# Performance work log

Hardware: AMD Instinct MI355X
Metric: run time of the kernel (lower is better)

The kernel has to match this reference:

```python
import jax, jax.numpy as jnp
import numpy as np

C_IN = 512      # backbone feature dim (din)
CORR = 256      # cfg.SIAMESE.NUM_CHANNELS_FOR_CORRELATION
EXPAND = 64     # expand_factor
N_ANCH = 9      # 3 scales x 3 ratios
KH = 7          # template spatial size
H = W = 32      # target feature map size
N_T = 2         # number of templates
BN_EPS = 1e-5


def _conv(x, w, b=None, pad=0, groups=1):
    out = jax.lax.conv_general_dilated(
        x, w, window_strides=(1, 1), padding=[(pad, pad), (pad, pad)],
        dimension_numbers=('NCHW', 'OIHW', 'NCHW'), feature_group_count=groups)
    if b is not None:
        out = out + b[None, :, None, None]
    return out


def setup_inputs() -> dict:
    key = jax.random.key(0)
    ks = jax.random.split(key, 10)
    return {
        'target_feat': jax.random.normal(ks[0], (1, C_IN, H, W), jnp.float32),
        'template_feat': jax.random.normal(ks[1], (N_T, C_IN, KH, KH), jnp.float32),
        'w_target': jax.random.normal(ks[2], (CORR, C_IN, 3, 3), jnp.float32) * 0.01,
        'b_target': jnp.zeros((CORR,), jnp.float32),
        'bn_gamma': jnp.ones((CORR,), jnp.float32),
        'bn_beta': jnp.zeros((CORR,), jnp.float32),
        'bn_mean': jax.random.normal(ks[3], (CORR,), jnp.float32) * 0.1,
        'bn_var': jax.random.uniform(ks[4], (CORR,), jnp.float32, 0.5, 1.5),
        'w_template': jax.random.normal(ks[5], (CORR * EXPAND, C_IN, 3, 3), jnp.float32) * 0.01,
        'b_template': jnp.zeros((CORR * EXPAND,), jnp.float32),
        'w_merge_cls': jax.random.normal(ks[6], (CORR,), jnp.float32) * 0.01,
        'corr_bias': jnp.zeros((EXPAND, 1, 1), jnp.float32),
        'w_cls': jax.random.normal(ks[7], (2 * N_ANCH, EXPAND, 1, 1), jnp.float32) * 0.01,
        'b_cls': jnp.zeros((2 * N_ANCH,), jnp.float32),
        'w_box': jax.random.normal(ks[8], (4 * N_ANCH, EXPAND, 1, 1), jnp.float32) * 0.001,
        'b_box': jnp.zeros((4 * N_ANCH,), jnp.float32),
    }


def reference(target_feat, template_feat, w_target, b_target, bn_gamma, bn_beta,
              bn_mean, bn_var, w_template, b_template, w_merge_cls, corr_bias,
              w_cls, b_cls, w_box, b_box):
    N = template_feat.shape[0]
    Hh, Ww = target_feat.shape[2], target_feat.shape[3]
    # RPN_Conv_target (3x3, pad 1) + BatchNorm (eval mode, running stats)
    t = _conv(target_feat, w_target, b_target, pad=1)               # (1, CORR, H, W)
    scale = (bn_gamma / jnp.sqrt(bn_var + BN_EPS))[None, :, None, None]
    t = (t - bn_mean[None, :, None, None]) * scale + bn_beta[None, :, None, None]
    # RPN_Conv_template (3x3, pad 1) on template features
    z = _conv(template_feat, w_template, b_template, pad=1)          # (N, CORR*EXPAND, kh, kw)
    kh, kw = z.shape[2], z.shape[3]
    # depth-wise cross correlation: kernel (N*EXPAND*CORR, 1, kh, kw), groups=CORR
    kern = z.reshape(N * EXPAND * CORR, 1, kh, kw)
    out = 0.1 * _conv(t, kern, pad=(kh - 1) // 2, groups=CORR)       # (1, N*EXPAND*CORR, H, W)
    out = out.reshape(N * EXPAND, CORR, Hh, Ww)
    # conv_merge_1x1_cls: 1x1 conv CORR -> 1, no bias
    out = jnp.einsum('nchw,c->nhw', out, w_merge_cls)                # (N*EXPAND, H, W)
    rpn_feat = out.reshape(N, EXPAND, Hh, Ww) + corr_bias[None]      # (N, 64, H, W)
    # cls / bbox heads (1x1 convs)
    cls = _conv(rpn_feat, w_cls, b_cls)                              # (N, 18, H, W)
    box = _conv(rpn_feat, w_box, b_box)                              # (N, 36, H, W)
    nc = cls.shape[1]
    # reshape to (N, 2, A*H, W), softmax over dim 1, reshape back
    prob = jax.nn.softmax(cls.reshape(N, 2, (nc // 2) * Hh, Ww), axis=1)
    prob = prob.reshape(N, nc, Hh, Ww)
    return prob, box
```

## Files before the change

### kernel.cpp

```cpp
#include <hip/hip_runtime.h>
#include <math.h>


#define WS_TFP 0
#define WS_WT  591872
#define WS_TP  1771520
#define WS_WF  2160640
#define WS_BF  2750464
#define WS_Z2P 2750592
#define WS_MRG 3152000

typedef float f4u __attribute__((ext_vector_type(4), aligned(4)));

__global__ __launch_bounds__(256) void k_fold(
    const float* __restrict__ wtpl,
    const float* __restrict__ wm,
    float* ws)
{
  const int g = blockIdx.x / 9, chunk = blockIdx.x % 9;
  const int tid = threadIdx.x;
  const int t = tid & 127, grp = tid >> 7;
  const int c0 = chunk * 512 + t * 4;
  const float* base = wtpl + (size_t)(g * 128 + grp * 64) * 4608 + c0;
  const float* wmb = wm + (g & 1) * 128 + grp * 64;
  float4 acc = make_float4(0.f, 0.f, 0.f, 0.f);
  for (int r = 0; r < 64; r += 8) {
    const float4 v0 = *(const float4*)(base + (size_t)(r + 0) * 4608);
    const float4 v1 = *(const float4*)(base + (size_t)(r + 1) * 4608);
    const float4 v2 = *(const float4*)(base + (size_t)(r + 2) * 4608);
    const float4 v3 = *(const float4*)(base + (size_t)(r + 3) * 4608);
    const float4 v4 = *(const float4*)(base + (size_t)(r + 4) * 4608);
    const float4 v5 = *(const float4*)(base + (size_t)(r + 5) * 4608);
    const float4 v6 = *(const float4*)(base + (size_t)(r + 6) * 4608);
    const float4 v7 = *(const float4*)(base + (size_t)(r + 7) * 4608);
    const float w0 = wmb[r + 0], w1 = wmb[r + 1], w2 = wmb[r + 2], w3 = wmb[r + 3];
    const float w4 = wmb[r + 4], w5 = wmb[r + 5], w6 = wmb[r + 6], w7 = wmb[r + 7];
    acc.x = fmaf(w0, v0.x, acc.x); acc.y = fmaf(w0, v0.y, acc.y);
    acc.z = fmaf(w0, v0.z, acc.z); acc.w = fmaf(w0, v0.w, acc.w);
    acc.x = fmaf(w1, v1.x, acc.x); acc.y = fmaf(w1, v1.y, acc.y);
    acc.z = fmaf(w1, v1.z, acc.z); acc.w = fmaf(w1, v1.w, acc.w);
    acc.x = fmaf(w2, v2.x, acc.x); acc.y = fmaf(w2, v2.y, acc.y);
    acc.z = fmaf(w2, v2.z, acc.z); acc.w = fmaf(w2, v2.w, acc.w);
    acc.x = fmaf(w3, v3.x, acc.x); acc.y = fmaf(w3, v3.y, acc.y);
    acc.z = fmaf(w3, v3.z, acc.z); acc.w = fmaf(w3, v3.w, acc.w);
    acc.x = fmaf(w4, v4.x, acc.x); acc.y = fmaf(w4, v4.y, acc.y);
    acc.z = fmaf(w4, v4.z, acc.z); acc.w = fmaf(w4, v4.w, acc.w);
    acc.x = fmaf(w5, v5.x, acc.x); acc.y = fmaf(w5, v5.y, acc.y);
    acc.z = fmaf(w5, v5.z, acc.z); acc.w = fmaf(w5, v5.w, acc.w);
    acc.x = fmaf(w6, v6.x, acc.x); acc.y = fmaf(w6, v6.y, acc.y);
    acc.z = fmaf(w6, v6.z, acc.z); acc.w = fmaf(w6, v6.w, acc.w);
    acc.x = fmaf(w7, v7.x, acc.x); acc.y = fmaf(w7, v7.y, acc.y);
    acc.z = fmaf(w7, v7.z, acc.z); acc.w = fmaf(w7, v7.w, acc.w);
  }
  __shared__ float4 red[128];
  if (grp) red[t] = acc;
  __syncthreads();
  if (!grp) {
    const float4 o = red[t];
    acc.x += o.x; acc.y += o.y; acc.z += o.z; acc.w += o.w;
    float* wf = ws + WS_WF;
    wf[(size_t)(c0 + 0) * 128 + g] = acc.x;
    wf[(size_t)(c0 + 1) * 128 + g] = acc.y;
    wf[(size_t)(c0 + 2) * 128 + g] = acc.z;
    wf[(size_t)(c0 + 3) * 128 + g] = acc.w;
  }
}

__global__ __launch_bounds__(256) void k0_prep(
    const float* __restrict__ tfeat,
    const float* __restrict__ wm,
    const float* __restrict__ btpl,
    float* ws)
{
  const int N0 = 591872, N2 = 389120;
  const int total = N0 + N2;
  for (int idx = blockIdx.x * 256 + threadIdx.x; idx < total + 128; idx += gridDim.x * 256) {
    if (idx < N0) {
      int ci = idx / 1156, r = idx % 1156;
      int yy = r / 34, xx = r % 34;
      float v = 0.f;
      if (yy >= 1 && yy <= 32 && xx >= 1 && xx <= 32)
        v = tfeat[ci * 1024 + (yy - 1) * 32 + (xx - 1)];
      ws[WS_TFP + idx] = v;
    } else if (idx < total) {
      ws[WS_TP + (idx - N0)] = 0.f;
    } else {
      const int eh = idx - total;
      const int e = eh >> 1, h = eh & 1;
      const float* wmp = wm + h * 128;
      const float* bp = btpl + e * 256 + h * 128;
      float s = 0.f;
      for (int cl = 0; cl < 128; cl++) s = fmaf(wmp[cl], bp[cl], s);
      ws[WS_BF + eh] = s;
    }
  }
}

__global__ __launch_bounds__(512) void k_conv(
    const float* __restrict__ wtgt,
    const float* __restrict__ btgt,
    const float* __restrict__ gamma, const float* __restrict__ beta,
    const float* __restrict__ mean, const float* __restrict__ var,
    float* ws)
{
  __shared__ float red[3][128][8];
  const int tid = threadIdx.x;
  const int ks = tid >> 7;
  const int sub = tid & 127;
  const int cog = sub >> 5;
  const int pxg = sub & 31;
  const int row = pxg >> 4;
  const int x0 = (pxg & 15) * 2;
  const int co0 = (blockIdx.x >> 4) * 16 + cog * 4;
  const int y = (blockIdx.x & 15) * 2 + row;
  const float* tfp = ws + WS_TFP;

  float acc[4][2] = {{0.f, 0.f}, {0.f, 0.f}, {0.f, 0.f}, {0.f, 0.f}};
  for (int i = 0; i < 128; i++) {
    const int ci = ks * 128 + i;
    const float* tin = tfp + (size_t)ci * 1156 + y * 34 + x0;
    const f4u p0 = *(const f4u*)(tin);
    const f4u p1 = *(const f4u*)(tin + 34);
    const f4u p2 = *(const f4u*)(tin + 68);
    #pragma unroll
    for (int c = 0; c < 4; c++) {
      const float* wr = wtgt + (size_t)(co0 + c) * 4608 + ci * 9;
      const f4u wa = *(const f4u*)(wr);
      const f4u wb = *(const f4u*)(wr + 4);
      const float w8 = wr[8];
      acc[c][0] += wa.x * p0.x + wa.y * p0.y + wa.z * p0.z
                 + wa.w * p1.x + wb.x * p1.y + wb.y * p1.z
                 + wb.z * p2.x + wb.w * p2.y + w8 * p2.z;
      acc[c][1] += wa.x * p0.y + wa.y * p0.z + wa.z * p0.w
                 + wa.w * p1.y + wb.x * p1.z + wb.y * p1.w
                 + wb.z * p2.y + wb.w * p2.z + w8 * p2.w;
    }
  }
  if (ks) {
    #pragma unroll
    for (int c = 0; c < 4; c++) {
      red[ks - 1][sub][c * 2 + 0] = acc[c][0];
      red[ks - 1][sub][c * 2 + 1] = acc[c][1];
    }
  }
  __syncthreads();
  if (ks == 0) {
    float* tP = ws + WS_TP;
    #pragma unroll
    for (int c = 0; c < 4; c++) {
      const int co = co0 + c;
      const float sc = gamma[co] * rsqrtf(var[co] + 1e-5f);
      #pragma unroll
      for (int p = 0; p < 2; p++) {
        float a = acc[c][p] + red[0][sub][c * 2 + p]
                            + red[1][sub][c * 2 + p]
                            + red[2][sub][c * 2 + p];
        float t = (a + btgt[co] - mean[co]) * sc + beta[co];
        t *= 0.1f;
        tP[co * 1520 + (y + 3) * 40 + (x0 + p + 3)] = t;
      }
    }
  }
}

__global__ __launch_bounds__(256) void k2_z2(
    const float* __restrict__ zfeat,
    float* ws)
{
  __shared__ float Tl[50][144];
  const int tid = threadIdx.x;
  const int n = blockIdx.x >> 5, kc = blockIdx.x & 31;
  const int ci0 = kc * 16;
  for (int idx = tid; idx < 7200; idx += 256) {
    const int uv = idx / 144, kk = idx % 144;
    float v = 0.f;
    if (uv < 49) {
      const int u = uv / 7, vv = uv % 7;
      const int ci = ci0 + kk / 9, pq = kk % 9;
      const int p = pq / 3, q = pq % 3;
      const int yy = u + p - 1, xx = vv + q - 1;
      if (yy >= 0 && yy < 7 && xx >= 0 && xx < 7)
        v = zfeat[n * 25088 + ci * 49 + yy * 7 + xx];
    }
    Tl[uv][kk] = v;
  }
  __syncthreads();
  const int ehq = tid & 31, uvg = tid >> 5;
  const int eh0 = ehq * 4;
  const int uv0 = (uvg == 0) ? 0 : uvg * 6 + 1;
  const float* wf = ws + WS_WF;
  float4 acc[7];
  #pragma unroll
  for (int i = 0; i < 7; i++) acc[i] = make_float4(0.f, 0.f, 0.f, 0.f);
  for (int g = 0; g < 36; g++) {
    const float* wr = wf + (size_t)(ci0 * 9 + g * 4) * 128 + eh0;
    const float4 wv0 = *(const float4*)(wr);
    const float4 wv1 = *(const float4*)(wr + 128);
    const float4 wv2 = *(const float4*)(wr + 256);
    const float4 wv3 = *(const float4*)(wr + 384);
    #pragma unroll
    for (int uu = 0; uu < 7; uu++) {
      const float4 t4 = *(const float4*)(&Tl[uv0 + uu][g * 4]);
      acc[uu].x = fmaf(t4.x, wv0.x, fmaf(t4.y, wv1.x, fmaf(t4.z, wv2.x, fmaf(t4.w, wv3.x, acc[uu].x))));
      acc[uu].y = fmaf(t4.x, wv0.y, fmaf(t4.y, wv1.y, fmaf(t4.z, wv2.y, fmaf(t4.w, wv3.y, acc[uu].y))));
      acc[uu].z = fmaf(t4.x, wv0.z, fmaf(t4.y, wv1.z, fmaf(t4.z, wv2.z, fmaf(t4.w, wv3.z, acc[uu].z))));
      acc[uu].w = fmaf(t4.x, wv0.w, fmaf(t4.y, wv1.w, fmaf(t4.z, wv2.w, fmaf(t4.w, wv3.w, acc[uu].w))));
    }
  }
  float* z2p = ws + WS_Z2P;
  #pragma unroll
  for (int uu = 0; uu < 7; uu++) {
    const int uv = uv0 + uu;
    if (uv <= 48)
      *(float4*)(z2p + ((size_t)((n * 32 + kc) * 49 + uv)) * 128 + eh0) = acc[uu];
  }
}

__global__ __launch_bounds__(128) void k3_merged(float* ws)
{
  __shared__ float Z2s[16][7][8];
  const int tid = threadIdx.x;
  const int bid = blockIdx.x;
  const int n = bid >> 7, rest = bid & 127;
  const int ec = rest >> 4, hq = rest & 15;
  const int c0 = ec * 16, h0 = hq * 2;
  const float* z2p = ws + WS_Z2P;
  const float* bf = ws + WS_BF;
  for (int idx = tid; idx < 784; idx += 128) {
    const int cl = idx & 15, uv = idx >> 4;
    float s = bf[c0 + cl];
    const float* p = z2p + (size_t)(n * 1568 + uv) * 128 + (c0 + cl);
    #pragma unroll 8
    for (int kc = 0; kc < 32; kc++) s += p[(size_t)kc * 6272];
    Z2s[cl][uv / 7][uv % 7] = s;
  }
  for (int idx = tid; idx < 112; idx += 128)
    Z2s[idx / 7][idx % 7][7] = 0.f;
  __syncthreads();

  const int e = tid >> 4, row = (tid >> 3) & 1, wq = tid & 7;
  const int w0 = wq * 4;
  const float* tP = ws + WS_TP;
  float acc[4] = {0.f, 0.f, 0.f, 0.f};
  #pragma unroll
  for (int h128 = 0; h128 < 2; h128++) {
    const int cl = 2 * e + h128;
    const float* tc = tP + (size_t)(128 * n + c0 + cl) * 1520;
    #pragma unroll
    for (int u = 0; u < 7; u++) {
      const float* trow = tc + (h0 + row + u) * 40 + w0;
      float tw[12];
      *(float4*)&tw[0] = *(const float4*)(trow);
      *(float4*)&tw[4] = *(const float4*)(trow + 4);
      *(float4*)&tw[8] = *(const float4*)(trow + 8);
      float z[8];
      *(float4*)&z[0] = *(const float4*)&Z2s[cl][u][0];
      *(float4*)&z[4] = *(const float4*)&Z2s[cl][u][4];
      #pragma unroll
      for (int px = 0; px < 4; px++)
        #pragma unroll
        for (int v = 0; v < 8; v++)
          acc[px] = fmaf(z[v], tw[px + v], acc[px]);
    }
  }
  float* mrg = ws + WS_MRG;
  *(float4*)(mrg + (size_t)(((n * 64 + ec * 8 + e) * 32) + h0 + row) * 32 + w0) =
      make_float4(acc[0], acc[1], acc[2], acc[3]);
}

__global__ __launch_bounds__(256) void k4_heads(
    const float* __restrict__ cb,
    const float* __restrict__ wcls, const float* __restrict__ bcls,
    const float* __restrict__ wbox, const float* __restrict__ bbox,
    float* ws, float* __restrict__ out)
{
  __shared__ float mrg_l[32][66];
  __shared__ float wcb_l[54][64];
  __shared__ float bias_l[54];
  __shared__ float logits[18][32];
  const int tid = threadIdx.x;
  const int n = blockIdx.x >> 5, h = blockIdx.x & 31;
  const float* mrg = ws + WS_MRG;
  for (int idx = tid; idx < 2048; idx += 256) {
    const int e = idx >> 5, w = idx & 31;
    mrg_l[w][e] = mrg[(size_t)(((n * 64 + e) * 32) + h) * 32 + w] + cb[e];
  }
  for (int idx = tid; idx < 3456; idx += 256) {
    const int ch = idx >> 6, e = idx & 63;
    wcb_l[ch][e] = (ch < 18) ? wcls[ch * 64 + e] : wbox[(ch - 18) * 64 + e];
  }
  if (tid < 54) bias_l[tid] = (tid < 18) ? bcls[tid] : bbox[tid - 18];
  __syncthreads();

  const int w = tid & 31, chg = tid >> 5;
  const int cnt = (chg < 6) ? 7 : 6;
  float acc[7] = {0.f, 0.f, 0.f, 0.f, 0.f, 0.f, 0.f};
  for (int e2 = 0; e2 < 32; e2++) {
    const float2 m2 = *(const float2*)&mrg_l[w][e2 * 2];
    #pragma unroll
    for (int i = 0; i < 7; i++) {
      if (i < cnt) {
        const int ch = chg + 8 * i;
        const float2 wv = *(const float2*)&wcb_l[ch][e2 * 2];
        acc[i] = fmaf(m2.x, wv.x, acc[i]);
        acc[i] = fmaf(m2.y, wv.y, acc[i]);
      }
    }
  }
  #pragma unroll
  for (int i = 0; i < 7; i++) {
    if (i < cnt) {
      const int ch = chg + 8 * i;
      const float v = acc[i] + bias_l[ch];
      if (ch < 18) logits[ch][w] = v;
      else out[36864 + n * 36864 + (ch - 18) * 1024 + h * 32 + w] = v;
    }
  }
  __syncthreads();
  for (int idx = tid; idx < 576; idx += 256) {
    const int ch = idx >> 5, w2 = idx & 31;
    const float a = logits[ch][w2];
    const float b = logits[(ch + 9) % 18][w2];
    const float m = fmaxf(a, b);
    const float ea = expf(a - m), eb = expf(b - m);
    out[n * 18432 + ch * 1024 + h * 32 + w2] = ea / (ea + eb);
  }
}

extern "C" void kernel_launch(void* const* d_in, const int* in_sizes, int n_in,
                              void* d_out, int out_size, void* d_ws, size_t ws_size,
                              hipStream_t stream) {
  (void)in_sizes; (void)n_in; (void)out_size; (void)ws_size;
  const float* target_feat   = (const float*)d_in[0];
  const float* template_feat = (const float*)d_in[1];
  const float* w_target      = (const float*)d_in[2];
  const float* b_target      = (const float*)d_in[3];
  const float* bn_gamma      = (const float*)d_in[4];
  const float* bn_beta       = (const float*)d_in[5];
  const float* bn_mean       = (const float*)d_in[6];
  const float* bn_var        = (const float*)d_in[7];
  const float* w_template    = (const float*)d_in[8];
  const float* b_template    = (const float*)d_in[9];
  const float* w_merge       = (const float*)d_in[10];
  const float* corr_bias     = (const float*)d_in[11];
  const float* w_cls         = (const float*)d_in[12];
  const float* b_cls         = (const float*)d_in[13];
  const float* w_box         = (const float*)d_in[14];
  const float* b_box         = (const float*)d_in[15];
  float* ws = (float*)d_ws;
  float* out = (float*)d_out;

  hipLaunchKernelGGL(k_fold, dim3(1152), dim3(256), 0, stream,
                     w_template, w_merge, ws);
  hipLaunchKernelGGL(k0_prep, dim3(2048), dim3(256), 0, stream,
                     target_feat, w_merge, b_template, ws);
  hipLaunchKernelGGL(k_conv, dim3(256), dim3(512), 0, stream,
                     w_target, b_target, bn_gamma, bn_beta, bn_mean, bn_var, ws);
  hipLaunchKernelGGL(k2_z2, dim3(64), dim3(256), 0, stream,
                     template_feat, ws);
  hipLaunchKernelGGL(k3_merged, dim3(256), dim3(128), 0, stream, ws);
  hipLaunchKernelGGL(k4_heads, dim3(64), dim3(256), 0, stream,
                     corr_bias, w_cls, b_cls, w_box, b_box, ws, out);
}
```

Before: 231.5 us.

## Split-K the target conv and template fold across more blocks with partial-sum buffers

The target 3x3 conv moves from 256 blocks, each reducing all 512 input channels, to 2048 blocks that each handle a 64-channel slice. Partials go to 16 global buffers, and a new k_cred kernel sums them and applies BatchNorm. k_fold is likewise split into two row halves written to separate buffers, which k2_z2 adds together on load. The aim is better GPU occupancy for work that was under-parallelized, at the cost of extra global partial-sum traffic and one more kernel launch.

```diff
diff --git a/kernel.cpp b/kernel.cpp
--- a/kernel.cpp
+++ b/kernel.cpp
@@ -3,66 +3,78 @@
 
 
 #define WS_TFP 0
-#define WS_WT  591872
-#define WS_TP  1771520
-#define WS_WF  2160640
-#define WS_BF  2750464
-#define WS_Z2P 2750592
-#define WS_MRG 3152000
+#define WS_TP  591872
+#define WS_BF  980992
+#define WS_WFP 981120
+#define WS_Z2P 2160768
+#define WS_MRG 2562176
+#define WS_CVP 2693248
+#define WFP_HALF 589824
 
 typedef float f4u __attribute__((ext_vector_type(4), aligned(4)));
+
+#define FMA4(ww, vv) \
+  acc.x = fmaf(ww, (vv).x, acc.x); acc.y = fmaf(ww, (vv).y, acc.y); \
+  acc.z = fmaf(ww, (vv).z, acc.z); acc.w = fmaf(ww, (vv).w, acc.w)
 
 __global__ __launch_bounds__(256) void k_fold(
     const float* __restrict__ wtpl,
     const float* __restrict__ wm,
     float* ws)
 {
-  const int g = blockIdx.x / 9, chunk = blockIdx.x % 9;
-  const int tid = threadIdx.x;
-  const int t = tid & 127, grp = tid >> 7;
-  const int c0 = chunk * 512 + t * 4;
-  const float* base = wtpl + (size_t)(g * 128 + grp * 64) * 4608 + c0;
-  const float* wmb = wm + (g & 1) * 128 + grp * 64;
+  const int bid = blockIdx.x;
+  const int g = bid / 18, rest = bid % 18;
+  const int chunk = rest >> 1, half = rest & 1;
+  const int tid = threadIdx.x;
+  const int colv = tid & 127, rowg = tid >> 7;
+  const int c0 = chunk * 512 + colv * 4;
+  const int row0 = g * 128 + half * 64 + rowg * 32;
+  const float* base = wtpl + (size_t)row0 * 4608 + c0;
+  const float* wmb = wm + (g & 1) * 128 + half * 64 + rowg * 32;
   float4 acc = make_float4(0.f, 0.f, 0.f, 0.f);
-  for (int r = 0; r < 64; r += 8) {
-    const float4 v0 = *(const float4*)(base + (size_t)(r + 0) * 4608);
-    const float4 v1 = *(const float4*)(base + (size_t)(r + 1) * 4608);
-    const float4 v2 = *(const float4*)(base + (size_t)(r + 2) * 4608);
-    const float4 v3 = *(const float4*)(base + (size_t)(r + 3) * 4608);
-    const float4 v4 = *(const float4*)(base + (size_t)(r + 4) * 4608);
-    const float4 v5 = *(const float4*)(base + (size_t)(r + 5) * 4608);
-    const float4 v6 = *(const float4*)(base + (size_t)(r + 6) * 4608);
-    const float4 v7 = *(const float4*)(base + (size_t)(r + 7) * 4608);
-    const float w0 = wmb[r + 0], w1 = wmb[r + 1], w2 = wmb[r + 2], w3 = wmb[r + 3];
-    const float w4 = wmb[r + 4], w5 = wmb[r + 5], w6 = wmb[r + 6], w7 = wmb[r + 7];
-    acc.x = fmaf(w0, v0.x, acc.x); acc.y = fmaf(w0, v0.y, acc.y);
-    acc.z = fmaf(w0, v0.z, acc.z); acc.w = fmaf(w0, v0.w, acc.w);
-    acc.x = fmaf(w1, v1.x, acc.x); acc.y = fmaf(w1, v1.y, acc.y);
-    acc.z = fmaf(w1, v1.z, acc.z); acc.w = fmaf(w1, v1.w, acc.w);
-    acc.x = fmaf(w2, v2.x, acc.x); acc.y = fmaf(w2, v2.y, acc.y);
-    acc.z = fmaf(w2, v2.z, acc.z); acc.w = fmaf(w2, v2.w, acc.w);
-    acc.x = fmaf(w3, v3.x, acc.x); acc.y = fmaf(w3, v3.y, acc.y);
-    acc.z = fmaf(w3, v3.z, acc.z); acc.w = fmaf(w3, v3.w, acc.w);
-    acc.x = fmaf(w4, v4.x, acc.x); acc.y = fmaf(w4, v4.y, acc.y);
-    acc.z = fmaf(w4, v4.z, acc.z); acc.w = fmaf(w4, v4.w, acc.w);
-    acc.x = fmaf(w5, v5.x, acc.x); acc.y = fmaf(w5, v5.y, acc.y);
-    acc.z = fmaf(w5, v5.z, acc.z); acc.w = fmaf(w5, v5.w, acc.w);
-    acc.x = fmaf(w6, v6.x, acc.x); acc.y = fmaf(w6, v6.y, acc.y);
-    acc.z = fmaf(w6, v6.z, acc.z); acc.w = fmaf(w6, v6.w, acc.w);
-    acc.x = fmaf(w7, v7.x, acc.x); acc.y = fmaf(w7, v7.y, acc.y);
-    acc.z = fmaf(w7, v7.z, acc.z); acc.w = fmaf(w7, v7.w, acc.w);
+  #pragma unroll
+  for (int rr = 0; rr < 32; rr += 16) {
+    const float* b = base + (size_t)rr * 4608;
+    const float4 v0  = *(const float4*)(b);
+    const float4 v1  = *(const float4*)(b + 1 * 4608);
+    const float4 v2  = *(const float4*)(b + 2 * 4608);
+    const float4 v3  = *(const float4*)(b + 3 * 4608);
+    const float4 v4  = *(const float4*)(b + 4 * 4608);
+    const float4 v5  = *(const float4*)(b + 5 * 4608);
+    const float4 v6  = *(const float4*)(b + 6 * 4608);
+    const float4 v7  = *(const float4*)(b + 7 * 4608);
+    const float4 v8  = *(const float4*)(b + 8 * 4608);
+    const float4 v9  = *(const float4*)(b + 9 * 4608);
+    const float4 v10 = *(const float4*)(b + 10 * 4608);
+    const float4 v11 = *(const float4*)(b + 11 * 4608);
+    const float4 v12 = *(const float4*)(b + 12 * 4608);
+    const float4 v13 = *(const float4*)(b + 13 * 4608);
+    const float4 v14 = *(const float4*)(b + 14 * 4608);
+    const float4 v15 = *(const float4*)(b + 15 * 4608);
+    const float w0 = wmb[rr + 0],  w1 = wmb[rr + 1];
+    const float w2 = wmb[rr + 2],  w3 = wmb[rr + 3];
+    const float w4 = wmb[rr + 4],  w5 = wmb[rr + 5];
+    const float w6 = wmb[rr + 6],  w7 = wmb[rr + 7];
+    const float w8 = wmb[rr + 8],  w9 = wmb[rr + 9];
+    const float w10 = wmb[rr + 10], w11 = wmb[rr + 11];
+    const float w12 = wmb[rr + 12], w13 = wmb[rr + 13];
+    const float w14 = wmb[rr + 14], w15 = wmb[rr + 15];
+    FMA4(w0, v0);   FMA4(w1, v1);   FMA4(w2, v2);   FMA4(w3, v3);
+    FMA4(w4, v4);   FMA4(w5, v5);   FMA4(w6, v6);   FMA4(w7, v7);
+    FMA4(w8, v8);   FMA4(w9, v9);   FMA4(w10, v10); FMA4(w11, v11);
+    FMA4(w12, v12); FMA4(w13, v13); FMA4(w14, v14); FMA4(w15, v15);
   }
   __shared__ float4 red[128];
-  if (grp) red[t] = acc;
-  __syncthreads();
-  if (!grp) {
-    const float4 o = red[t];
+  if (rowg) red[colv] = acc;
+  __syncthreads();
+  if (!rowg) {
+    const float4 o = red[colv];
     acc.x += o.x; acc.y += o.y; acc.z += o.z; acc.w += o.w;
-    float* wf = ws + WS_WF;
-    wf[(size_t)(c0 + 0) * 128 + g] = acc.x;
-    wf[(size_t)(c0 + 1) * 128 + g] = acc.y;
-    wf[(size_t)(c0 + 2) * 128 + g] = acc.z;
-    wf[(size_t)(c0 + 3) * 128 + g] = acc.w;
+    float* wp = ws + WS_WFP + (size_t)half * WFP_HALF;
+    wp[(size_t)(c0 + 0) * 128 + g] = acc.x;
+    wp[(size_t)(c0 + 1) * 128 + g] = acc.y;
+    wp[(size_t)(c0 + 2) * 128 + g] = acc.z;
+    wp[(size_t)(c0 + 3) * 128 + g] = acc.w;
   }
 }
 
@@ -96,28 +108,24 @@
   }
 }
 
-__global__ __launch_bounds__(512) void k_conv(
+__global__ __launch_bounds__(256) void k_conv(
     const float* __restrict__ wtgt,
-    const float* __restrict__ btgt,
-    const float* __restrict__ gamma, const float* __restrict__ beta,
-    const float* __restrict__ mean, const float* __restrict__ var,
-    float* ws)
-{
-  __shared__ float red[3][128][8];
-  const int tid = threadIdx.x;
-  const int ks = tid >> 7;
-  const int sub = tid & 127;
-  const int cog = sub >> 5;
-  const int pxg = sub & 31;
-  const int row = pxg >> 4;
-  const int x0 = (pxg & 15) * 2;
-  const int co0 = (blockIdx.x >> 4) * 16 + cog * 4;
-  const int y = (blockIdx.x & 15) * 2 + row;
+    float* ws)
+{
+  const int bid = blockIdx.x;
+  const int coblk = bid >> 7, pxblk = (bid >> 3) & 15, ks = bid & 7;
+  const int tid = threadIdx.x;
+  const int ksub = tid >> 7, sub = tid & 127;
+  const int cog = sub >> 5, pxg = sub & 31;
+  const int row = pxg >> 4, x0 = (pxg & 15) * 2;
+  const int y = pxblk * 2 + row;
+  const int co0 = coblk * 16 + cog * 4;
+  const int ci0 = ks * 64 + ksub * 32;
   const float* tfp = ws + WS_TFP;
 
   float acc[4][2] = {{0.f, 0.f}, {0.f, 0.f}, {0.f, 0.f}, {0.f, 0.f}};
-  for (int i = 0; i < 128; i++) {
-    const int ci = ks * 128 + i;
+  for (int i = 0; i < 32; i++) {
+    const int ci = ci0 + i;
     const float* tin = tfp + (size_t)ci * 1156 + y * 34 + x0;
     const f4u p0 = *(const f4u*)(tin);
     const f4u p1 = *(const f4u*)(tin + 34);
@@ -136,30 +144,36 @@
                  + wb.z * p2.y + wb.w * p2.z + w8 * p2.w;
     }
   }
-  if (ks) {
-    #pragma unroll
-    for (int c = 0; c < 4; c++) {
-      red[ks - 1][sub][c * 2 + 0] = acc[c][0];
-      red[ks - 1][sub][c * 2 + 1] = acc[c][1];
-    }
-  }
-  __syncthreads();
-  if (ks == 0) {
-    float* tP = ws + WS_TP;
-    #pragma unroll
-    for (int c = 0; c < 4; c++) {
-      const int co = co0 + c;
-      const float sc = gamma[co] * rsqrtf(var[co] + 1e-5f);
-      #pragma unroll
-      for (int p = 0; p < 2; p++) {
-        float a = acc[c][p] + red[0][sub][c * 2 + p]
-                            + red[1][sub][c * 2 + p]
-                            + red[2][sub][c * 2 + p];
-        float t = (a + btgt[co] - mean[co]) * sc + beta[co];
-        t *= 0.1f;
-        tP[co * 1520 + (y + 3) * 40 + (x0 + p + 3)] = t;
-      }
-    }
+  float* cvp = ws + WS_CVP + (size_t)(ks * 2 + ksub) * 262144;
+  #pragma unroll
+  for (int c = 0; c < 4; c++) {
+    cvp[(co0 + c) * 1024 + y * 32 + x0 + 0] = acc[c][0];
+    cvp[(co0 + c) * 1024 + y * 32 + x0 + 1] = acc[c][1];
+  }
+}
+
+__global__ __launch_bounds__(256) void k_cred(
+    const float* __restrict__ btgt,
+    const float* __restrict__ gamma, const float* __restrict__ beta,
+    const float* __restrict__ mean, const float* __restrict__ var,
+    float* ws)
+{
+  const int co = blockIdx.x;
+  const int tid = threadIdx.x;
+  const float sc = gamma[co] * rsqrtf(var[co] + 1e-5f);
+  const float off = btgt[co] - mean[co];
+  const float bt = beta[co];
+  const float* cvp = ws + WS_CVP + (size_t)co * 1024;
+  float* tP = ws + WS_TP;
+  #pragma unroll
+  for (int k = 0; k < 4; k++) {
+    const int j = k * 256 + tid;
+    float s = 0.f;
+    #pragma unroll
+    for (int sl = 0; sl < 16; sl++) s += cvp[(size_t)sl * 262144 + j];
+    const float t = ((s + off) * sc + bt) * 0.1f;
+    const int yy = j >> 5, xx = j & 31;
+    tP[co * 1520 + (yy + 3) * 40 + (xx + 3)] = t;
   }
 }
 
@@ -188,16 +202,25 @@
   const int ehq = tid & 31, uvg = tid >> 5;
   const int eh0 = ehq * 4;
   const int uv0 = (uvg == 0) ? 0 : uvg * 6 + 1;
-  const float* wf = ws + WS_WF;
+  const float* wfp = ws + WS_WFP;
   float4 acc[7];
   #pragma unroll
   for (int i = 0; i < 7; i++) acc[i] = make_float4(0.f, 0.f, 0.f, 0.f);
   for (int g = 0; g < 36; g++) {
-    const float* wr = wf + (size_t)(ci0 * 9 + g * 4) * 128 + eh0;
-    const float4 wv0 = *(const float4*)(wr);
-    const float4 wv1 = *(const float4*)(wr + 128);
-    const float4 wv2 = *(const float4*)(wr + 256);
-    const float4 wv3 = *(const float4*)(wr + 384);
+    const float* wr = wfp + (size_t)(ci0 * 9 + g * 4) * 128 + eh0;
+    const float* wr2 = wr + WFP_HALF;
+    float4 wv0 = *(const float4*)(wr);
+    float4 wv1 = *(const float4*)(wr + 128);
+    float4 wv2 = *(const float4*)(wr + 256);
+    float4 wv3 = *(const float4*)(wr + 384);
+    const float4 u0 = *(const float4*)(wr2);
+    const float4 u1 = *(const float4*)(wr2 + 128);
+    const float4 u2 = *(const float4*)(wr2 + 256);
+    const float4 u3 = *(const float4*)(wr2 + 384);
+    wv0.x += u0.x; wv0.y += u0.y; wv0.z += u0.z; wv0.w += u0.w;
+    wv1.x += u1.x; wv1.y += u1.y; wv1.z += u1.z; wv1.w += u1.w;
+    wv2.x += u2.x; wv2.y += u2.y; wv2.z += u2.z; wv2.w += u2.w;
+    wv3.x += u3.x; wv3.y += u3.y; wv3.z += u3.z; wv3.w += u3.w;
     #pragma unroll
     for (int uu = 0; uu < 7; uu++) {
       const float4 t4 = *(const float4*)(&Tl[uv0 + uu][g * 4]);
@@ -350,12 +373,14 @@
   float* ws = (float*)d_ws;
   float* out = (float*)d_out;
 
-  hipLaunchKernelGGL(k_fold, dim3(1152), dim3(256), 0, stream,
+  hipLaunchKernelGGL(k_fold, dim3(2304), dim3(256), 0, stream,
                      w_template, w_merge, ws);
   hipLaunchKernelGGL(k0_prep, dim3(2048), dim3(256), 0, stream,
                      target_feat, w_merge, b_template, ws);
-  hipLaunchKernelGGL(k_conv, dim3(256), dim3(512), 0, stream,
-                     w_target, b_target, bn_gamma, bn_beta, bn_mean, bn_var, ws);
+  hipLaunchKernelGGL(k_conv, dim3(2048), dim3(256), 0, stream,
+                     w_target, ws);
+  hipLaunchKernelGGL(k_cred, dim3(256), dim3(256), 0, stream,
+                     b_target, bn_gamma, bn_beta, bn_mean, bn_var, ws);
   hipLaunchKernelGGL(k2_z2, dim3(64), dim3(256), 0, stream,
                      template_feat, ws);
   hipLaunchKernelGGL(k3_merged, dim3(256), dim3(128), 0, stream, ws);
```

Measured after the change: 229.7 us. About the same (-0.8%).
